# Optimization experiments

Measured on AMD Instinct MI355X. Metric: run time of the kernel, lower is better.

Reference implementation:

```python
import jax, jax.numpy as jnp
import numpy as np

D_MODEL = 768
N_HEADS = 12
HEAD_DIM = D_MODEL // N_HEADS
B, L = 2, 4096


def setup_inputs() -> dict:
    key = jax.random.key(0)
    ks = jax.random.split(key, 11)
    s = 0.02
    inp = {
        "q": jax.random.normal(ks[0], (B, L, D_MODEL), jnp.float32),
        "k": jax.random.normal(ks[1], (B, L, D_MODEL), jnp.float32),
        "v": jax.random.normal(ks[2], (B, L, D_MODEL), jnp.float32),
        # causal mask: True = masked (matches torch masked_fill semantics)
        "mask": jnp.triu(jnp.ones((L, L), bool), k=1)[None, None, :, :],
        "wq": jax.random.normal(ks[3], (D_MODEL, D_MODEL), jnp.float32) * s,
        "bq": jnp.zeros((D_MODEL,), jnp.float32),
        "wk": jax.random.normal(ks[4], (D_MODEL, D_MODEL), jnp.float32) * s,
        "bk": jnp.zeros((D_MODEL,), jnp.float32),
        "wv": jax.random.normal(ks[5], (D_MODEL, D_MODEL), jnp.float32) * s,
        "bv": jnp.zeros((D_MODEL,), jnp.float32),
        "wo": jax.random.normal(ks[6], (D_MODEL, D_MODEL), jnp.float32) * s,
        "bo": jnp.zeros((D_MODEL,), jnp.float32),
    }
    return inp


def reference(q, k, v, mask, wq, bq, wk, bk, wv, bv, wo, bo):
    Bs, Ls, Ds = q.shape

    def split_heads(x):  # [B,L,D] -> [B,H,L,hd]
        return x.reshape(Bs, -1, N_HEADS, HEAD_DIM).transpose(0, 2, 1, 3)

    qh = split_heads(q @ wq.T + bq)
    kh = split_heads(k @ wk.T + bk)
    vh = split_heads(v @ wv.T + bv)

    scores = jnp.einsum("bhqd,bhkd->bhqk", qh, kh) / jnp.sqrt(
        jnp.asarray(HEAD_DIM, qh.dtype)
    )
    scores = jnp.where(mask, -jnp.inf, scores)
    attn = jax.nn.softmax(scores, axis=-1)
    out = jnp.einsum("bhqk,bhkd->bhqd", attn, vh)  # [B,H,L,hd]
    out = out.transpose(0, 2, 1, 3).reshape(Bs, Ls, Ds)
    return out @ wo.T + bo
```

## Files before the change

### kernel.cpp

```cpp
#include <hip/hip_runtime.h>
#include <hip/hip_bf16.h>
#include <stdint.h>

#define DM 768
#define NH 12
#define HD 64
#define BB 2
#define LL 4096
#define BH (BB*NH)
#define ML (BB*LL)

typedef short bf16x8 __attribute__((ext_vector_type(8)));
typedef short bf16x4 __attribute__((ext_vector_type(4)));
typedef float f32x4 __attribute__((ext_vector_type(4)));

#define LOG2E 1.4426950408889634f

__device__ inline short f2b(float f) {
  __hip_bfloat16 h = __float2bfloat16(f);
  return *reinterpret_cast<short*>(&h);
}

__device__ inline void gll16(const void* g, void* l) {
  __builtin_amdgcn_global_load_lds(
      (const __attribute__((address_space(1))) unsigned int*)g,
      (__attribute__((address_space(3))) unsigned int*)l, 16, 0, 0);
}

__global__ __launch_bounds__(256) void convx_kernel(
    const float* __restrict__ src, short* __restrict__ dst)
{
  size_t i = ((size_t)blockIdx.x * 256 + threadIdx.x) * 8;
  float4 a = *(const float4*)(src + i);
  float4 b = *(const float4*)(src + i + 4);
  bf16x8 r = {f2b(a.x), f2b(a.y), f2b(a.z), f2b(a.w),
              f2b(b.x), f2b(b.y), f2b(b.z), f2b(b.w)};
  *(bf16x8*)(dst + i) = r;
}

__global__ __launch_bounds__(256) void convx3_kernel(
    const float* __restrict__ s0, const float* __restrict__ s1,
    const float* __restrict__ s2, short* __restrict__ d0,
    short* __restrict__ d1, short* __restrict__ d2)
{
  const float* src = blockIdx.y == 0 ? s0 : (blockIdx.y == 1 ? s1 : s2);
  short*       dst = blockIdx.y == 0 ? d0 : (blockIdx.y == 1 ? d1 : d2);
  size_t i = ((size_t)blockIdx.x * 256 + threadIdx.x) * 8;
  float4 a = *(const float4*)(src + i);
  float4 b = *(const float4*)(src + i + 4);
  bf16x8 r = {f2b(a.x), f2b(a.y), f2b(a.z), f2b(a.w),
              f2b(b.x), f2b(b.y), f2b(b.z), f2b(b.w)};
  *(bf16x8*)(dst + i) = r;
}

__global__ __launch_bounds__(256) void convw_kernel(
    const float* __restrict__ w0, const float* __restrict__ w1,
    const float* __restrict__ w2, const float* __restrict__ w3,
    short* __restrict__ o0, short* __restrict__ o1,
    short* __restrict__ o2, short* __restrict__ o3)
{
  const float* src; short* dst;
  switch (blockIdx.y) {
    case 0: src = w0; dst = o0; break;
    case 1: src = w1; dst = o1; break;
    case 2: src = w2; dst = o2; break;
    default: src = w3; dst = o3; break;
  }
  size_t i = ((size_t)blockIdx.x * 256 + threadIdx.x) * 8;
  float4 a = *(const float4*)(src + i);
  float4 b = *(const float4*)(src + i + 4);
  bf16x8 r = {f2b(a.x), f2b(a.y), f2b(a.z), f2b(a.w),
              f2b(b.x), f2b(b.y), f2b(b.z), f2b(b.w)};
  *(bf16x8*)(dst + i) = r;
}

struct GemmAcc { f32x4 a[4][2]; };

__device__ inline void gemm_core(
    const short* __restrict__ A, const short* __restrict__ Bw,
    int m0, int n0, short* abuf0, short* abuf1, short* bbuf0, short* bbuf1,
    GemmAcc& G)
{
  const int lane = threadIdx.x & 63;
  const int w    = threadIdx.x >> 6;
  const int g    = lane >> 4;
  const int mr   = lane & 15;
  const int wr   = w >> 1;
  const int wc   = w & 1;
  const int srow = lane >> 3;
  const int scol = ((lane & 7) ^ srow) * 8;

  short* abuf[2] = {abuf0, abuf1};
  short* bbuf[2] = {bbuf0, bbuf1};

  #pragma unroll
  for (int i = 0; i < 4; ++i)
    gll16(A + (size_t)(m0 + w * 32 + i * 8 + srow) * DM + scol,
          (char*)abuf[0] + (w * 32 + i * 8) * 128);
  #pragma unroll
  for (int i = 0; i < 2; ++i)
    gll16(Bw + (size_t)(n0 + w * 16 + i * 8 + srow) * DM + scol,
          (char*)bbuf[0] + (w * 16 + i * 8) * 128);

  const int nk = DM / 64;
  for (int t = 0; t < nk; ++t) {
    __syncthreads();
    if (t + 1 < nk) {
      const int k1 = (t + 1) * 64;
      #pragma unroll
      for (int i = 0; i < 4; ++i)
        gll16(A + (size_t)(m0 + w * 32 + i * 8 + srow) * DM + k1 + scol,
              (char*)abuf[(t + 1) & 1] + (w * 32 + i * 8) * 128);
      #pragma unroll
      for (int i = 0; i < 2; ++i)
        gll16(Bw + (size_t)(n0 + w * 16 + i * 8 + srow) * DM + k1 + scol,
              (char*)bbuf[(t + 1) & 1] + (w * 16 + i * 8) * 128);
    }
    const char* ab = (const char*)abuf[t & 1];
    const char* bb = (const char*)bbuf[t & 1];
    #pragma unroll
    for (int ks = 0; ks < 2; ++ks) {
      const int chunk = ((ks * 4 + g) ^ (mr & 7)) * 16;
      bf16x8 af[4], bfr[2];
      #pragma unroll
      for (int m = 0; m < 4; ++m)
        af[m] = *(const bf16x8*)(ab + (wr * 64 + m * 16 + mr) * 128 + chunk);
      #pragma unroll
      for (int nf = 0; nf < 2; ++nf)
        bfr[nf] = *(const bf16x8*)(bb + (wc * 32 + nf * 16 + mr) * 128 + chunk);
      #pragma unroll
      for (int m = 0; m < 4; ++m)
        #pragma unroll
        for (int nf = 0; nf < 2; ++nf)
          G.a[m][nf] = __builtin_amdgcn_mfma_f32_16x16x32_bf16(af[m], bfr[nf], G.a[m][nf], 0, 0, 0);
    }
  }
}

__device__ inline void gemm_epi_bf16(
    GemmAcc& G, const float* __restrict__ bias, short* __restrict__ out,
    int m0, int n0, float scale, bool vmode)
{
  const int lane = threadIdx.x & 63;
  const int w    = threadIdx.x >> 6;
  const int g    = lane >> 4;
  const int mr   = lane & 15;
  const int wr   = w >> 1;
  const int wc   = w & 1;
  #pragma unroll
  for (int nf = 0; nf < 2; ++nf) {
    const int col = n0 + wc * 32 + nf * 16 + mr;
    const float bv = bias[col];
    const int h = col >> 6, c = col & 63;
    #pragma unroll
    for (int m = 0; m < 4; ++m)
      #pragma unroll
      for (int r = 0; r < 4; ++r) {
        const int row = m0 + wr * 64 + m * 16 + g * 4 + r;
        const int b = row >> 12, li = row & 4095;
        const float val = (G.a[m][nf][r] + bv) * scale;
        size_t idx;
        if (vmode) idx = ((size_t)(b * NH + h) * HD + c) * LL + li;
        else       idx = ((size_t)(b * NH + h) * LL + li) * HD + c;
        out[idx] = f2b(val);
      }
  }
}

__global__ __launch_bounds__(256) void qkv_gemm_kernel(
    const short* __restrict__ xq, const short* __restrict__ xk,
    const short* __restrict__ xv, const short* __restrict__ wqb,
    const short* __restrict__ wkb, const short* __restrict__ wvb,
    const float* __restrict__ bq, const float* __restrict__ bk,
    const float* __restrict__ bv, short* __restrict__ qh,
    short* __restrict__ kh, short* __restrict__ vt)
{
  __shared__ __align__(16) short abuf[2][128 * 64];
  __shared__ __align__(16) short bbuf[2][64 * 64];
  const int z = blockIdx.z;
  const short* A  = z == 0 ? xq : (z == 1 ? xk : xv);
  const short* Bw = z == 0 ? wqb : (z == 1 ? wkb : wvb);
  const float* bi = z == 0 ? bq : (z == 1 ? bk : bv);
  short* out      = z == 0 ? qh : (z == 1 ? kh : vt);
  const float scale = z == 0 ? 0.125f * LOG2E : 1.0f;
  const int m0 = blockIdx.x * 128;
  const int n0 = blockIdx.y * 64;

  GemmAcc G = {};
  gemm_core(A, Bw, m0, n0, abuf[0], abuf[1], bbuf[0], bbuf[1], G);
  gemm_epi_bf16(G, bi, out, m0, n0, scale, z == 2);
}

template<int MODE>
__global__ __launch_bounds__(256) void proj_gemm_kernel(
    const short* __restrict__ A, const short* __restrict__ Bw,
    const float* __restrict__ bias, short* __restrict__ out, float scale)
{
  __shared__ __align__(16) short abuf[2][128 * 64];
  __shared__ __align__(16) short bbuf[2][64 * 64];
  const int m0 = blockIdx.x * 128;
  const int n0 = blockIdx.y * 64;
  GemmAcc G = {};
  gemm_core(A, Bw, m0, n0, abuf[0], abuf[1], bbuf[0], bbuf[1], G);
  gemm_epi_bf16(G, bias, out, m0, n0, scale, MODE == 2);
}

__global__ __launch_bounds__(256) void outproj_kernel(
    const short* __restrict__ A, const short* __restrict__ Bw,
    const float* __restrict__ bias, float* __restrict__ out)
{
  __shared__ __align__(16) short abuf[2][128 * 64];
  __shared__ __align__(16) short bbuf[2][64 * 64];
  const int m0 = blockIdx.x * 128;
  const int n0 = blockIdx.y * 64;
  GemmAcc G = {};
  gemm_core(A, Bw, m0, n0, abuf[0], abuf[1], bbuf[0], bbuf[1], G);

  const int lane = threadIdx.x & 63;
  const int w    = threadIdx.x >> 6;
  const int g    = lane >> 4;
  const int mr   = lane & 15;
  const int wr   = w >> 1;
  const int wc   = w & 1;
  #pragma unroll
  for (int nf = 0; nf < 2; ++nf) {
    const int col = n0 + wc * 32 + nf * 16 + mr;
    const float bv = bias[col];
    #pragma unroll
    for (int m = 0; m < 4; ++m)
      #pragma unroll
      for (int r = 0; r < 4; ++r) {
        const int row = m0 + wr * 64 + m * 16 + g * 4 + r;
        out[(size_t)row * DM + col] = G.a[m][nf][r] + bv;
      }
  }
}

__global__ __launch_bounds__(256) void attn_kernel(
    const short* __restrict__ qh, const short* __restrict__ kh,
    const short* __restrict__ vt, short* __restrict__ attn_out)
{
  __shared__ __align__(16) char kbuf[2][8192];
  __shared__ __align__(16) char vbuf[2][8192];
  __shared__ __align__(16) char plds[4][2048];

  const int bh   = blockIdx.y;
  const int lane = threadIdx.x & 63;
  const int w    = threadIdx.x >> 6;
  const int g    = lane >> 4;
  const int mr   = lane & 15;

  const short* qp = qh + (size_t)bh * LL * HD;
  const short* kp = kh + (size_t)bh * LL * HD;
  const short* vp = vt + (size_t)bh * HD * LL;
  char* wbase = plds[w];

  int wroff[4], rdoff[2];
  #pragma unroll
  for (int mf = 0; mf < 4; ++mf)
    wroff[mf] = mr * 128 + ((mf * 32 + g * 8) ^ ((mr & 7) << 4));
  #pragma unroll
  for (int c = 0; c < 2; ++c)
    rdoff[c] = mr * 128 + ((c * 64 + g * 16) ^ ((mr & 7) << 4));
  const int swz = (mr & 7) << 4;
  const int ssub = lane >> 3;
  const int scol = ((lane & 7) ^ ssub) * 8;

  const int b = bh / NH, h = bh % NH;

  #pragma unroll
  for (int ph = 0; ph < 2; ++ph) {
    const int qtile = ph == 0 ? (63 - (int)blockIdx.x) : (int)blockIdx.x;
    const int q0blk = qtile * 64;
    const int q0w   = q0blk + w * 16;
    const int nt    = qtile + 1;

    if (ph == 1) __syncthreads();

    const short* qrow = qp + (size_t)(q0w + mr) * HD + g * 8;
    bf16x8 qb0 = *(const bf16x8*)qrow;
    bf16x8 qb1 = *(const bf16x8*)(qrow + 32);

    f32x4 acc[4] = {};
    float lreg = 0.f;

    #pragma unroll
    for (int p = 0; p < 2; ++p) {
      const int row = p * 32 + w * 8 + ssub;
      gll16(kp + (size_t)row * HD + scol, kbuf[0] + p * 4096 + w * 1024);
      gll16(vp + (size_t)row * LL + scol, vbuf[0] + p * 4096 + w * 1024);
    }

    for (int t = 0; t < nt; ++t) {
      __syncthreads();
      const int kv0 = t * 64;

      if (t + 1 < nt) {
        const int kv1 = kv0 + 64;
        char* kb = kbuf[(t + 1) & 1];
        char* vb = vbuf[(t + 1) & 1];
        #pragma unroll
        for (int p = 0; p < 2; ++p) {
          const int row = p * 32 + w * 8 + ssub;
          gll16(kp + (size_t)(kv1 + row) * HD + scol, kb + p * 4096 + w * 1024);
          gll16(vp + (size_t)row * LL + kv1 + scol, vb + p * 4096 + w * 1024);
        }
      }

      {
        const char* kb = kbuf[t & 1];
        const char* vb = vbuf[t & 1];

        f32x4 s[4] = {};
        #pragma unroll
        for (int mf = 0; mf < 4; ++mf) {
          const char* krow = kb + (mf * 16 + mr) * 128;
          bf16x8 ka0 = *(const bf16x8*)(krow + ((g * 16) ^ swz));
          bf16x8 ka1 = *(const bf16x8*)(krow + ((64 + g * 16) ^ swz));
          s[mf] = __builtin_amdgcn_mfma_f32_16x16x32_bf16(ka0, qb0, s[mf], 0, 0, 0);
          s[mf] = __builtin_amdgcn_mfma_f32_16x16x32_bf16(ka1, qb1, s[mf], 0, 0, 0);
        }

        if (kv0 + 63 > q0w) {
          #pragma unroll
          for (int mf = 0; mf < 4; ++mf)
            #pragma unroll
            for (int r = 0; r < 4; ++r)
              if (kv0 + mf * 16 + g * 4 + r > q0w + mr)
                s[mf][r] = -INFINITY;
        }

        float sa[4];
        #pragma unroll
        for (int mf = 0; mf < 4; ++mf) {
          #pragma unroll
          for (int r = 0; r < 4; ++r)
            s[mf][r] = exp2f(s[mf][r]);
          sa[mf] = (s[mf][0] + s[mf][1]) + (s[mf][2] + s[mf][3]);
        }
        float rs = (sa[0] + sa[1]) + (sa[2] + sa[3]);
        rs += __shfl_xor(rs, 16, 64);
        rs += __shfl_xor(rs, 32, 64);
        lreg += rs;

        #pragma unroll
        for (int mf = 0; mf < 4; ++mf) {
          bf16x4 w4 = {f2b(s[mf][0]), f2b(s[mf][1]), f2b(s[mf][2]), f2b(s[mf][3])};
          *(bf16x4*)(wbase + wroff[mf]) = w4;
        }

        #pragma unroll
        for (int c = 0; c < 2; ++c) {
          bf16x8 pb = *(const bf16x8*)(wbase + rdoff[c]);
          #pragma unroll
          for (int df = 0; df < 4; ++df) {
            const char* vrow = vb + (df * 16 + mr) * 128;
            bf16x8 av = *(const bf16x8*)(vrow + ((c * 64 + g * 16) ^ swz));
            acc[df] = __builtin_amdgcn_mfma_f32_16x16x32_bf16(av, pb, acc[df], 0, 0, 0);
          }
        }
      }
    }

    const float inv = 1.0f / lreg;
    const int q = q0w + mr;
    short* orow = attn_out + ((size_t)(b * LL + q)) * DM + h * HD + g * 4;
    #pragma unroll
    for (int df = 0; df < 4; ++df) {
      bf16x4 st = {f2b(acc[df][0] * inv), f2b(acc[df][1] * inv),
                   f2b(acc[df][2] * inv), f2b(acc[df][3] * inv)};
      *(bf16x4*)(orow + df * 16) = st;
    }
  }
}

extern "C" void kernel_launch(void* const* d_in, const int* in_sizes, int n_in,
                              void* d_out, int out_size, void* d_ws, size_t ws_size,
                              hipStream_t stream) {
  const float* q  = (const float*)d_in[0];
  const float* k  = (const float*)d_in[1];
  const float* v  = (const float*)d_in[2];
  const float* wq = (const float*)d_in[4];
  const float* bq = (const float*)d_in[5];
  const float* wk = (const float*)d_in[6];
  const float* bk = (const float*)d_in[7];
  const float* wv = (const float*)d_in[8];
  const float* bv = (const float*)d_in[9];
  const float* wo = (const float*)d_in[10];
  const float* bo = (const float*)d_in[11];

  const size_t S   = (size_t)BH * LL * HD;
  const size_t WSZ = (size_t)DM * DM;
  short* qh   = (short*)d_ws;
  short* kh   = qh + S;
  short* vt   = kh + S;
  short* attn = vt + S;
  short* wqb  = attn + S;
  short* wkb  = wqb + WSZ;
  short* wvb  = wkb + WSZ;
  short* wob  = wvb + WSZ;
  short* xtra = wob + WSZ;

  const size_t need_fused = (size_t)(6 * S + 4 * WSZ) * sizeof(short);
  const bool fused = ws_size >= need_fused;

  dim3 blk(256);
  convw_kernel<<<dim3(WSZ / 2048, 4), blk, 0, stream>>>(wq, wk, wv, wo, wqb, wkb, wvb, wob);
  dim3 ggemm(ML / 128, DM / 64);

  if (fused) {
    short* xbq = attn;
    short* xbk = xtra;
    short* xbv = xtra + S;
    convx3_kernel<<<dim3(S / 2048, 3), blk, 0, stream>>>(q, k, v, xbq, xbk, xbv);
    qkv_gemm_kernel<<<dim3(ML / 128, DM / 64, 3), blk, 0, stream>>>(
        xbq, xbk, xbv, wqb, wkb, wvb, bq, bk, bv, qh, kh, vt);
  } else {
    short* xb = attn;
    convx_kernel<<<dim3(S / 2048), blk, 0, stream>>>(q, xb);
    proj_gemm_kernel<0><<<ggemm, blk, 0, stream>>>(xb, wqb, bq, qh, 0.125f * LOG2E);
    convx_kernel<<<dim3(S / 2048), blk, 0, stream>>>(k, xb);
    proj_gemm_kernel<1><<<ggemm, blk, 0, stream>>>(xb, wkb, bk, kh, 1.0f);
    convx_kernel<<<dim3(S / 2048), blk, 0, stream>>>(v, xb);
    proj_gemm_kernel<2><<<ggemm, blk, 0, stream>>>(xb, wvb, bv, vt, 1.0f);
  }

  attn_kernel<<<dim3(32, BH), blk, 0, stream>>>(qh, kh, vt, attn);
  outproj_kernel<<<ggemm, blk, 0, stream>>>(attn, wob, bo, (float*)d_out);
}
```

Before: 382.1 us.

## Enlarge GEMM tiles to 128x128 with K=32 steps; defer softmax row-sum reduction

The projection GEMMs move from 128x64 output tiles with 64-wide K steps to 128x128 tiles with 32-wide K steps. Each wave now holds a 4x4 grid of MFMA accumulators, and the LDS swizzle is redone for 64-byte rows. The aim is more operand reuse per LDS load and fewer blocks, at the cost of more accumulator registers and twice as many K iterations and barriers. In the attention kernel, the per-tile row-sum cross-lane shuffles are replaced by a per-lane vector accumulator that is reduced once at the end.

```diff
diff --git a/kernel.cpp b/kernel.cpp
--- a/kernel.cpp
+++ b/kernel.cpp
@@ -74,96 +74,57 @@
   *(bf16x8*)(dst + i) = r;
 }
 
-struct GemmAcc { f32x4 a[4][2]; };
-
-__device__ inline void gemm_core(
+__device__ __forceinline__ void gemm128_core(
     const short* __restrict__ A, const short* __restrict__ Bw,
-    int m0, int n0, short* abuf0, short* abuf1, short* bbuf0, short* bbuf1,
-    GemmAcc& G)
-{
-  const int lane = threadIdx.x & 63;
-  const int w    = threadIdx.x >> 6;
-  const int g    = lane >> 4;
-  const int mr   = lane & 15;
-  const int wr   = w >> 1;
-  const int wc   = w & 1;
-  const int srow = lane >> 3;
-  const int scol = ((lane & 7) ^ srow) * 8;
-
-  short* abuf[2] = {abuf0, abuf1};
-  short* bbuf[2] = {bbuf0, bbuf1};
-
-  #pragma unroll
-  for (int i = 0; i < 4; ++i)
-    gll16(A + (size_t)(m0 + w * 32 + i * 8 + srow) * DM + scol,
-          (char*)abuf[0] + (w * 32 + i * 8) * 128);
-  #pragma unroll
-  for (int i = 0; i < 2; ++i)
-    gll16(Bw + (size_t)(n0 + w * 16 + i * 8 + srow) * DM + scol,
-          (char*)bbuf[0] + (w * 16 + i * 8) * 128);
-
-  const int nk = DM / 64;
+    int m0, int n0, char* ab0, char* ab1, char* bb0, char* bb1,
+    f32x4 (&acc)[4][4])
+{
+  const int lane   = threadIdx.x & 63;
+  const int w      = threadIdx.x >> 6;
+  const int g      = lane >> 4;
+  const int mr     = lane & 15;
+  const int wr     = w >> 1, wc = w & 1;
+  const int srow   = lane >> 2;
+  const int schunk = (lane & 3) ^ (srow & 3);
+  const int rdswz  = (mr & 3) << 4;
+
+  #pragma unroll
+  for (int i = 0; i < 2; ++i) {
+    gll16(A  + (size_t)(m0 + w * 32 + i * 16 + srow) * DM + schunk * 8,
+          ab0 + (w * 32 + i * 16) * 64);
+    gll16(Bw + (size_t)(n0 + w * 32 + i * 16 + srow) * DM + schunk * 8,
+          bb0 + (w * 32 + i * 16) * 64);
+  }
+
+  const int nk = DM / 32;
   for (int t = 0; t < nk; ++t) {
     __syncthreads();
     if (t + 1 < nk) {
-      const int k1 = (t + 1) * 64;
+      const int k1 = (t + 1) * 32;
+      char* an = ((t + 1) & 1) ? ab1 : ab0;
+      char* bn = ((t + 1) & 1) ? bb1 : bb0;
       #pragma unroll
-      for (int i = 0; i < 4; ++i)
-        gll16(A + (size_t)(m0 + w * 32 + i * 8 + srow) * DM + k1 + scol,
-              (char*)abuf[(t + 1) & 1] + (w * 32 + i * 8) * 128);
-      #pragma unroll
-      for (int i = 0; i < 2; ++i)
-        gll16(Bw + (size_t)(n0 + w * 16 + i * 8 + srow) * DM + k1 + scol,
-              (char*)bbuf[(t + 1) & 1] + (w * 16 + i * 8) * 128);
+      for (int i = 0; i < 2; ++i) {
+        gll16(A  + (size_t)(m0 + w * 32 + i * 16 + srow) * DM + k1 + schunk * 8,
+              an + (w * 32 + i * 16) * 64);
+        gll16(Bw + (size_t)(n0 + w * 32 + i * 16 + srow) * DM + k1 + schunk * 8,
+              bn + (w * 32 + i * 16) * 64);
+      }
     }
-    const char* ab = (const char*)abuf[t & 1];
-    const char* bb = (const char*)bbuf[t & 1];
-    #pragma unroll
-    for (int ks = 0; ks < 2; ++ks) {
-      const int chunk = ((ks * 4 + g) ^ (mr & 7)) * 16;
-      bf16x8 af[4], bfr[2];
-      #pragma unroll
-      for (int m = 0; m < 4; ++m)
-        af[m] = *(const bf16x8*)(ab + (wr * 64 + m * 16 + mr) * 128 + chunk);
-      #pragma unroll
-      for (int nf = 0; nf < 2; ++nf)
-        bfr[nf] = *(const bf16x8*)(bb + (wc * 32 + nf * 16 + mr) * 128 + chunk);
-      #pragma unroll
-      for (int m = 0; m < 4; ++m)
-        #pragma unroll
-        for (int nf = 0; nf < 2; ++nf)
-          G.a[m][nf] = __builtin_amdgcn_mfma_f32_16x16x32_bf16(af[m], bfr[nf], G.a[m][nf], 0, 0, 0);
-    }
-  }
-}
-
-__device__ inline void gemm_epi_bf16(
-    GemmAcc& G, const float* __restrict__ bias, short* __restrict__ out,
-    int m0, int n0, float scale, bool vmode)
-{
-  const int lane = threadIdx.x & 63;
-  const int w    = threadIdx.x >> 6;
-  const int g    = lane >> 4;
-  const int mr   = lane & 15;
-  const int wr   = w >> 1;
-  const int wc   = w & 1;
-  #pragma unroll
-  for (int nf = 0; nf < 2; ++nf) {
-    const int col = n0 + wc * 32 + nf * 16 + mr;
-    const float bv = bias[col];
-    const int h = col >> 6, c = col & 63;
+    const char* ac = (t & 1) ? ab1 : ab0;
+    const char* bc = (t & 1) ? bb1 : bb0;
+    bf16x8 af[4], bfr[4];
+    #pragma unroll
+    for (int m = 0; m < 4; ++m)
+      af[m] = *(const bf16x8*)(ac + (wr * 64 + m * 16 + mr) * 64 + ((g * 16) ^ rdswz));
+    #pragma unroll
+    for (int n = 0; n < 4; ++n)
+      bfr[n] = *(const bf16x8*)(bc + (wc * 64 + n * 16 + mr) * 64 + ((g * 16) ^ rdswz));
     #pragma unroll
     for (int m = 0; m < 4; ++m)
       #pragma unroll
-      for (int r = 0; r < 4; ++r) {
-        const int row = m0 + wr * 64 + m * 16 + g * 4 + r;
-        const int b = row >> 12, li = row & 4095;
-        const float val = (G.a[m][nf][r] + bv) * scale;
-        size_t idx;
-        if (vmode) idx = ((size_t)(b * NH + h) * HD + c) * LL + li;
-        else       idx = ((size_t)(b * NH + h) * LL + li) * HD + c;
-        out[idx] = f2b(val);
-      }
+      for (int n = 0; n < 4; ++n)
+        acc[m][n] = __builtin_amdgcn_mfma_f32_16x16x32_bf16(af[m], bfr[n], acc[m][n], 0, 0, 0);
   }
 }
 
@@ -175,20 +136,44 @@
     const float* __restrict__ bv, short* __restrict__ qh,
     short* __restrict__ kh, short* __restrict__ vt)
 {
-  __shared__ __align__(16) short abuf[2][128 * 64];
-  __shared__ __align__(16) short bbuf[2][64 * 64];
+  __shared__ __align__(16) char abuf[2][128 * 64];
+  __shared__ __align__(16) char bbuf[2][128 * 64];
   const int z = blockIdx.z;
   const short* A  = z == 0 ? xq : (z == 1 ? xk : xv);
   const short* Bw = z == 0 ? wqb : (z == 1 ? wkb : wvb);
   const float* bi = z == 0 ? bq : (z == 1 ? bk : bv);
   short* out      = z == 0 ? qh : (z == 1 ? kh : vt);
   const float scale = z == 0 ? 0.125f * LOG2E : 1.0f;
+  const bool vmode  = (z == 2);
   const int m0 = blockIdx.x * 128;
-  const int n0 = blockIdx.y * 64;
-
-  GemmAcc G = {};
-  gemm_core(A, Bw, m0, n0, abuf[0], abuf[1], bbuf[0], bbuf[1], G);
-  gemm_epi_bf16(G, bi, out, m0, n0, scale, z == 2);
+  const int n0 = blockIdx.y * 128;
+
+  f32x4 acc[4][4] = {};
+  gemm128_core(A, Bw, m0, n0, abuf[0], abuf[1], bbuf[0], bbuf[1], acc);
+
+  const int lane = threadIdx.x & 63;
+  const int w    = threadIdx.x >> 6;
+  const int g    = lane >> 4;
+  const int mr   = lane & 15;
+  const int wr   = w >> 1, wc = w & 1;
+  #pragma unroll
+  for (int nf = 0; nf < 4; ++nf) {
+    const int col = n0 + wc * 64 + nf * 16 + mr;
+    const float bv2 = bi[col];
+    const int h = col >> 6, c = col & 63;
+    #pragma unroll
+    for (int m = 0; m < 4; ++m)
+      #pragma unroll
+      for (int r = 0; r < 4; ++r) {
+        const int row = m0 + wr * 64 + m * 16 + g * 4 + r;
+        const int b = row >> 12, li = row & 4095;
+        const float val = (acc[m][nf][r] + bv2) * scale;
+        size_t idx;
+        if (vmode) idx = ((size_t)(b * NH + h) * HD + c) * LL + li;
+        else       idx = ((size_t)(b * NH + h) * LL + li) * HD + c;
+        out[idx] = f2b(val);
+      }
+  }
 }
 
 template<int MODE>
@@ -196,42 +181,64 @@
     const short* __restrict__ A, const short* __restrict__ Bw,
     const float* __restrict__ bias, short* __restrict__ out, float scale)
 {
-  __shared__ __align__(16) short abuf[2][128 * 64];
-  __shared__ __align__(16) short bbuf[2][64 * 64];
+  __shared__ __align__(16) char abuf[2][128 * 64];
+  __shared__ __align__(16) char bbuf[2][128 * 64];
   const int m0 = blockIdx.x * 128;
-  const int n0 = blockIdx.y * 64;
-  GemmAcc G = {};
-  gemm_core(A, Bw, m0, n0, abuf[0], abuf[1], bbuf[0], bbuf[1], G);
-  gemm_epi_bf16(G, bias, out, m0, n0, scale, MODE == 2);
-}
-
-__global__ __launch_bounds__(256) void outproj_kernel(
-    const short* __restrict__ A, const short* __restrict__ Bw,
-    const float* __restrict__ bias, float* __restrict__ out)
-{
-  __shared__ __align__(16) short abuf[2][128 * 64];
-  __shared__ __align__(16) short bbuf[2][64 * 64];
-  const int m0 = blockIdx.x * 128;
-  const int n0 = blockIdx.y * 64;
-  GemmAcc G = {};
-  gemm_core(A, Bw, m0, n0, abuf[0], abuf[1], bbuf[0], bbuf[1], G);
+  const int n0 = blockIdx.y * 128;
+  f32x4 acc[4][4] = {};
+  gemm128_core(A, Bw, m0, n0, abuf[0], abuf[1], bbuf[0], bbuf[1], acc);
 
   const int lane = threadIdx.x & 63;
   const int w    = threadIdx.x >> 6;
   const int g    = lane >> 4;
   const int mr   = lane & 15;
-  const int wr   = w >> 1;
-  const int wc   = w & 1;
-  #pragma unroll
-  for (int nf = 0; nf < 2; ++nf) {
-    const int col = n0 + wc * 32 + nf * 16 + mr;
+  const int wr   = w >> 1, wc = w & 1;
+  #pragma unroll
+  for (int nf = 0; nf < 4; ++nf) {
+    const int col = n0 + wc * 64 + nf * 16 + mr;
     const float bv = bias[col];
+    const int h = col >> 6, c = col & 63;
     #pragma unroll
     for (int m = 0; m < 4; ++m)
       #pragma unroll
       for (int r = 0; r < 4; ++r) {
         const int row = m0 + wr * 64 + m * 16 + g * 4 + r;
-        out[(size_t)row * DM + col] = G.a[m][nf][r] + bv;
+        const int b = row >> 12, li = row & 4095;
+        const float val = (acc[m][nf][r] + bv) * scale;
+        size_t idx;
+        if (MODE == 2) idx = ((size_t)(b * NH + h) * HD + c) * LL + li;
+        else           idx = ((size_t)(b * NH + h) * LL + li) * HD + c;
+        out[idx] = f2b(val);
+      }
+  }
+}
+
+__global__ __launch_bounds__(256) void outproj_kernel(
+    const short* __restrict__ A, const short* __restrict__ Bw,
+    const float* __restrict__ bias, float* __restrict__ out)
+{
+  __shared__ __align__(16) char abuf[2][128 * 64];
+  __shared__ __align__(16) char bbuf[2][128 * 64];
+  const int m0 = blockIdx.x * 128;
+  const int n0 = blockIdx.y * 128;
+  f32x4 acc[4][4] = {};
+  gemm128_core(A, Bw, m0, n0, abuf[0], abuf[1], bbuf[0], bbuf[1], acc);
+
+  const int lane = threadIdx.x & 63;
+  const int w    = threadIdx.x >> 6;
+  const int g    = lane >> 4;
+  const int mr   = lane & 15;
+  const int wr   = w >> 1, wc = w & 1;
+  #pragma unroll
+  for (int nf = 0; nf < 4; ++nf) {
+    const int col = n0 + wc * 64 + nf * 16 + mr;
+    const float bv = bias[col];
+    #pragma unroll
+    for (int m = 0; m < 4; ++m)
+      #pragma unroll
+      for (int r = 0; r < 4; ++r) {
+        const int row = m0 + wr * 64 + m * 16 + g * 4 + r;
+        out[(size_t)row * DM + col] = acc[m][nf][r] + bv;
       }
   }
 }
@@ -282,7 +289,7 @@
     bf16x8 qb1 = *(const bf16x8*)(qrow + 32);
 
     f32x4 acc[4] = {};
-    float lreg = 0.f;
+    f32x4 lsum = {0.f, 0.f, 0.f, 0.f};
 
     #pragma unroll
     for (int p = 0; p < 2; ++p) {
@@ -330,18 +337,13 @@
                 s[mf][r] = -INFINITY;
         }
 
-        float sa[4];
         #pragma unroll
         for (int mf = 0; mf < 4; ++mf) {
           #pragma unroll
           for (int r = 0; r < 4; ++r)
             s[mf][r] = exp2f(s[mf][r]);
-          sa[mf] = (s[mf][0] + s[mf][1]) + (s[mf][2] + s[mf][3]);
-        }
-        float rs = (sa[0] + sa[1]) + (sa[2] + sa[3]);
-        rs += __shfl_xor(rs, 16, 64);
-        rs += __shfl_xor(rs, 32, 64);
-        lreg += rs;
+          lsum += s[mf];
+        }
 
         #pragma unroll
         for (int mf = 0; mf < 4; ++mf) {
@@ -361,6 +363,10 @@
         }
       }
     }
+
+    float lreg = (lsum[0] + lsum[1]) + (lsum[2] + lsum[3]);
+    lreg += __shfl_xor(lreg, 16, 64);
+    lreg += __shfl_xor(lreg, 32, 64);
 
     const float inv = 1.0f / lreg;
     const int q = q0w + mr;
@@ -406,14 +412,14 @@
 
   dim3 blk(256);
   convw_kernel<<<dim3(WSZ / 2048, 4), blk, 0, stream>>>(wq, wk, wv, wo, wqb, wkb, wvb, wob);
-  dim3 ggemm(ML / 128, DM / 64);
+  dim3 ggemm(ML / 128, DM / 128);
 
   if (fused) {
     short* xbq = attn;
     short* xbk = xtra;
     short* xbv = xtra + S;
     convx3_kernel<<<dim3(S / 2048, 3), blk, 0, stream>>>(q, k, v, xbq, xbk, xbv);
-    qkv_gemm_kernel<<<dim3(ML / 128, DM / 64, 3), blk, 0, stream>>>(
+    qkv_gemm_kernel<<<dim3(ML / 128, DM / 128, 3), blk, 0, stream>>>(
         xbq, xbk, xbv, wqb, wkb, wvb, bq, bk, bv, qh, kh, vt);
   } else {
     short* xb = attn;
```

Measured after the change: 366.4 us. 1.04x faster.
